# Kernel optimization log

Hardware: AMD Instinct MI355X
Metric: run time of the kernel (lower is better)

The kernel has to match this reference:

```python
import jax, jax.numpy as jnp
import numpy as np

KNOW = 128
EXER_N = 20000
STU_N = 50000
N_EDGES = 1000000
N_EDGES_P = 950000
BATCH = 8192
SOFT_PARA = 0.2
EPS = 1e-8


def setup_inputs() -> dict:
    key = jax.random.key(0)
    ks = jax.random.split(key, 10)
    return {
        'stu_emb': jax.random.normal(ks[0], (STU_N, KNOW), jnp.float32) * 0.1,
        'exer_emb': jax.random.normal(ks[1], (EXER_N, KNOW), jnp.float32) * 0.1,
        'W_ue': jax.random.normal(ks[2], (KNOW, KNOW), jnp.float32) / np.sqrt(KNOW),
        'W_ue_per': jax.random.normal(ks[3], (KNOW, KNOW), jnp.float32) / np.sqrt(KNOW),
        'W_deep': jax.random.normal(ks[4], (KNOW, KNOW), jnp.float32) / np.sqrt(KNOW),
        'src_e': jax.random.randint(ks[5], (N_EDGES,), 0, EXER_N),
        'dst_e': jax.random.randint(ks[6], (N_EDGES,), 0, STU_N),
        'src_p': jax.random.randint(ks[7], (N_EDGES_P,), 0, EXER_N),
        'dst_p': jax.random.randint(ks[8], (N_EDGES_P,), 0, STU_N),
        'stu_id': jax.random.randint(ks[9], (BATCH,), 0, STU_N),
    }


def _graph_layer(exer, W, src, dst):
    # u_from_e: messages flow exercise -> student. Linear transform then mean-aggregate.
    msg = exer[src] @ W                                   # [E_edges, K]
    agg = jax.ops.segment_sum(msg, dst, num_segments=STU_N)
    deg = jax.ops.segment_sum(jnp.ones_like(dst, jnp.float32), dst, num_segments=STU_N)
    return agg / jnp.maximum(deg, 1.0)[:, None]           # [STU_N, K]


def reference(stu_emb, exer_emb, W_ue, W_ue_per, W_deep, src_e, dst_e, src_p, dst_p, stu_id):
    # ExpressionDooubleEva: two parallel graph views
    stu1 = stu_emb + _graph_layer(exer_emb, W_ue, src_e, dst_e)
    stu_per = stu_emb + _graph_layer(exer_emb, W_ue_per, src_p, dst_p)
    # ExpressionSingleEva (u_from_e output is overwritten by u_from_e_deep in source)
    stu2 = stu1 + _graph_layer(exer_emb, W_deep, src_e, dst_e)
    stu2_per = stu_per + _graph_layer(exer_emb, W_deep, src_e, dst_e)

    b1 = stu2[stu_id]          # [B, K]
    b2 = stu2_per[stu_id]      # [B, K]
    n1 = b1 / jnp.linalg.norm(b1, axis=1, keepdims=True)
    n2 = b2 / jnp.linalg.norm(b2, axis=1, keepdims=True)
    sim = (n1 @ n2.T) / SOFT_PARA                         # [B, B]
    # faithful to source: numerator = exp(diag(sim)), denominator = sum of RAW sim row
    diag_exp = jnp.exp(jnp.diagonal(sim))
    row_sum = jnp.sum(sim, axis=1)
    ratio = diag_exp / (row_sum + EPS)
    ssl_loss = jnp.mean(-jnp.log(jnp.maximum(ratio, EPS)))
    return stu2, ssl_loss
```

## Files before the change

### kernel.cpp

```cpp
#include <hip/hip_runtime.h>
#include <math.h>

#define KNOW 128
#define STU_N 50000
#define EXER_N 20000
#define BATCH 8192
#define NE 1000000
#define NEP 950000
#define SOFT_INV 5.0f
#define EPS 1e-8f

#define CAP 64
#define NBIN 256
#define SPB 196
#define SSE 4608
#define SSP 1536
#define P1B 256
#define P1T 1024

typedef unsigned short u16;
typedef unsigned int u32;

typedef __attribute__((ext_vector_type(8))) short bf16x8;
typedef __attribute__((ext_vector_type(4))) float f32x4;

__device__ __forceinline__ u16 f2bf(float f) {
  union { float f; u32 u; } v;
  v.f = f;
  u32 r = (v.u + 0x7FFFu + ((v.u >> 16) & 1u)) >> 16;
  return (u16)r;
}
__device__ __forceinline__ float bflo(u32 u) {
  union { u32 u; float f; } v;
  v.u = u << 16;
  return v.f;
}
__device__ __forceinline__ float bfhi(u32 u) {
  union { u32 u; float f; } v;
  v.u = u & 0xFFFF0000u;
  return v.f;
}
__device__ __forceinline__ float bfu(u16 h) {
  union { u32 u; float f; } v;
  v.u = ((u32)h) << 16;
  return v.f;
}

__global__ void set_flags(const int* __restrict__ stu_id,
                          unsigned char* __restrict__ flag,
                          int* __restrict__ gcur_e, int* __restrict__ gcur_p) {
  int i = blockIdx.x * blockDim.x + threadIdx.x;
  if (i < BATCH) flag[stu_id[i]] = 1;
  if (i < NBIN) {
    gcur_e[i] = i * SSE;
    gcur_p[i] = i * SSP;
  }
}

__global__ __launch_bounds__(P1T) void bin_pass1(
    const int* __restrict__ dst_e, const int* __restrict__ src_e,
    const int* __restrict__ dst_p, const int* __restrict__ src_p,
    const unsigned char* __restrict__ flag, int* __restrict__ gcur_e,
    int* __restrict__ gcur_p, u32* __restrict__ stag_e,
    u32* __restrict__ stag_p) {
  __shared__ int cntE[NBIN], cntP[NBIN];
  __shared__ int baseE[NBIN], baseP[NBIN];
  __shared__ int curE[NBIN], curP[NBIN];
  int t = threadIdx.x;
  if (t < NBIN) {
    cntE[t] = 0;
    cntP[t] = 0;
  }
  __syncthreads();
  int b = blockIdx.x;
  int e0 = (int)((long long)NE * b / P1B);
  int e1 = (int)((long long)NE * (b + 1) / P1B);
  int p0 = (int)((long long)NEP * b / P1B);
  int p1 = (int)((long long)NEP * (b + 1) / P1B);
  for (int i = e0 + t; i < e1; i += P1T) {
    int d = __builtin_nontemporal_load(&dst_e[i]);
    atomicAdd(&cntE[d / SPB], 1);
  }
  for (int i = p0 + t; i < p1; i += P1T) {
    int d = __builtin_nontemporal_load(&dst_p[i]);
    if (flag[d]) atomicAdd(&cntP[d / SPB], 1);
  }
  __syncthreads();
  if (t < NBIN) {
    baseE[t] = atomicAdd(&gcur_e[t], cntE[t]);
    baseP[t] = atomicAdd(&gcur_p[t], cntP[t]);
    curE[t] = 0;
    curP[t] = 0;
  }
  __syncthreads();
  for (int i = e0 + t; i < e1; i += P1T) {
    int d = __builtin_nontemporal_load(&dst_e[i]);
    int s = __builtin_nontemporal_load(&src_e[i]);
    int bin = d / SPB;
    int pos = baseE[bin] + atomicAdd(&curE[bin], 1);
    if (pos < (bin + 1) * SSE)
      stag_e[pos] = ((u32)(d - bin * SPB) << 16) | (u32)s;
  }
  for (int i = p0 + t; i < p1; i += P1T) {
    int d = __builtin_nontemporal_load(&dst_p[i]);
    if (!flag[d]) continue;
    int s = __builtin_nontemporal_load(&src_p[i]);
    int bin = d / SPB;
    int pos = baseP[bin] + atomicAdd(&curP[bin], 1);
    if (pos < (bin + 1) * SSP)
      stag_p[pos] = ((u32)(d - bin * SPB) << 16) | (u32)s;
  }
}

__global__ __launch_bounds__(256) void bin_pass2(
    const u32* __restrict__ stag_e, const u32* __restrict__ stag_p,
    const int* __restrict__ gcur_e, const int* __restrict__ gcur_p,
    u16* __restrict__ bucket_e, u16* __restrict__ bucket_p,
    int* __restrict__ cnt_e, int* __restrict__ cnt_p) {
  __shared__ u16 be[SPB * CAP];
  __shared__ u16 bp[SPB * CAP];
  __shared__ int ce[SPB], cp[SPB];
  int t = threadIdx.x;
  int bin = blockIdx.x;
  for (int i = t; i < SPB; i += 256) {
    ce[i] = 0;
    cp[i] = 0;
  }
  __syncthreads();
  int ne = gcur_e[bin] - bin * SSE;
  if (ne > SSE) ne = SSE;
  int np = gcur_p[bin] - bin * SSP;
  if (np > SSP) np = SSP;
  const u32* se = stag_e + (size_t)bin * SSE;
  for (int i = t; i < ne; i += 256) {
    u32 w = se[i];
    int dl = (int)(w >> 16), s = (int)(w & 0xFFFFu);
    int slot = atomicAdd(&ce[dl], 1);
    if (slot < CAP) be[dl * CAP + slot] = (u16)s;
  }
  const u32* sp = stag_p + (size_t)bin * SSP;
  for (int i = t; i < np; i += 256) {
    u32 w = sp[i];
    int dl = (int)(w >> 16), s = (int)(w & 0xFFFFu);
    int slot = atomicAdd(&cp[dl], 1);
    if (slot < CAP) bp[dl * CAP + slot] = (u16)s;
  }
  __syncthreads();
  int s0 = bin * SPB;
  int nstu = STU_N - s0;
  if (nstu > SPB) nstu = SPB;
  if (nstu <= 0) return;
  int nvec = nstu * CAP * 2 / 16;
  const uint4* bev = (const uint4*)be;
  uint4* ge = (uint4*)(bucket_e + (size_t)s0 * CAP);
  for (int i = t; i < nvec; i += 256) ge[i] = bev[i];
  const uint4* bpv = (const uint4*)bp;
  uint4* gp = (uint4*)(bucket_p + (size_t)s0 * CAP);
  for (int i = t; i < nvec; i += 256) gp[i] = bpv[i];
  for (int i = t; i < nstu; i += 256) {
    cnt_e[s0 + i] = ce[i];
    cnt_p[s0 + i] = cp[i];
  }
}

#define BM_T 80

#define SPL(dh, dl, i, x)                 \
  {                                       \
    u16 _hb = f2bf(x);                    \
    float _hf = bfu(_hb);                 \
    dh[i] = (short)_hb;                   \
    dl[i] = (short)f2bf((x) - _hf);       \
  }

__global__ __launch_bounds__(256) void transform_mfma(
    const float* __restrict__ exer, const float* __restrict__ W_ue,
    const float* __restrict__ W_per, const float* __restrict__ W_deep,
    u16* __restrict__ X_sum, u16* __restrict__ X_per,
    u16* __restrict__ X_deep) {
  __shared__ u16 wt_hi[KNOW * KNOW];
  __shared__ u16 wt_lo[KNOW * KNOW];
  int t = threadIdx.x;
  int which = blockIdx.y;
  u16* outp = (which == 0) ? X_sum : (which == 1) ? X_per : X_deep;

  {
    int c = t & 127;
    int rbase = (t >> 7) * 64;
    int swz = (c & 7) << 4;
    for (int r = rbase; r < rbase + 64; r += 2) {
      float w0, w1;
      if (which == 0) {
        w0 = W_ue[r * KNOW + c] + W_deep[r * KNOW + c];
        w1 = W_ue[(r + 1) * KNOW + c] + W_deep[(r + 1) * KNOW + c];
      } else {
        const float* Ws = (which == 1) ? W_per : W_deep;
        w0 = Ws[r * KNOW + c];
        w1 = Ws[(r + 1) * KNOW + c];
      }
      u16 h0 = f2bf(w0);
      u16 l0 = f2bf(w0 - bfu(h0));
      u16 h1 = f2bf(w1);
      u16 l1 = f2bf(w1 - bfu(h1));
      int bo = c * 256 + ((r * 2) ^ swz);
      *(u32*)((char*)wt_hi + bo) = (u32)h0 | ((u32)h1 << 16);
      *(u32*)((char*)wt_lo + bo) = (u32)l0 | ((u32)l1 << 16);
    }
  }
  __syncthreads();

  int wv = t >> 6;
  int l = t & 63;
  int bn = l & 15;
  int kb = l >> 4;

  bf16x8 bh[2][4], bl[2][4];
#pragma unroll
  for (int nt = 0; nt < 2; ++nt) {
    int n = wv * 32 + nt * 16 + bn;
    int rb = n * 256;
    int swz = (n & 7) << 4;
#pragma unroll
    for (int ks = 0; ks < 4; ++ks) {
      int bo = rb + (((ks * 32 + kb * 8) * 2) ^ swz);
      bh[nt][ks] = *(const bf16x8*)((const char*)wt_hi + bo);
      bl[nt][ks] = *(const bf16x8*)((const char*)wt_lo + bo);
    }
  }

  int row0 = blockIdx.x * BM_T;
#pragma unroll 1
  for (int rt = 0; rt < 5; ++rt) {
    const float* ep = exer + (size_t)(row0 + rt * 16 + bn) * KNOW;
    f32x4 acc0 = {0.f, 0.f, 0.f, 0.f};
    f32x4 acc1 = {0.f, 0.f, 0.f, 0.f};
#pragma unroll
    for (int ks = 0; ks < 4; ++ks) {
      float4 a0 = *(const float4*)(ep + ks * 32 + kb * 8);
      float4 a1 = *(const float4*)(ep + ks * 32 + kb * 8 + 4);
      bf16x8 ah, al;
      SPL(ah, al, 0, a0.x)
      SPL(ah, al, 1, a0.y)
      SPL(ah, al, 2, a0.z)
      SPL(ah, al, 3, a0.w)
      SPL(ah, al, 4, a1.x)
      SPL(ah, al, 5, a1.y)
      SPL(ah, al, 6, a1.z)
      SPL(ah, al, 7, a1.w)
      acc0 = __builtin_amdgcn_mfma_f32_16x16x32_bf16(ah, bh[0][ks], acc0, 0, 0, 0);
      acc0 = __builtin_amdgcn_mfma_f32_16x16x32_bf16(al, bh[0][ks], acc0, 0, 0, 0);
      acc0 = __builtin_amdgcn_mfma_f32_16x16x32_bf16(ah, bl[0][ks], acc0, 0, 0, 0);
      acc1 = __builtin_amdgcn_mfma_f32_16x16x32_bf16(ah, bh[1][ks], acc1, 0, 0, 0);
      acc1 = __builtin_amdgcn_mfma_f32_16x16x32_bf16(al, bh[1][ks], acc1, 0, 0, 0);
      acc1 = __builtin_amdgcn_mfma_f32_16x16x32_bf16(ah, bl[1][ks], acc1, 0, 0, 0);
    }
    int orow = row0 + rt * 16 + kb * 4;
    int oc = wv * 32 + bn;
#pragma unroll
    for (int r = 0; r < 4; ++r) {
      outp[(size_t)(orow + r) * KNOW + oc] = f2bf(acc0[r]);
      outp[(size_t)(orow + r) * KNOW + oc + 16] = f2bf(acc1[r]);
    }
  }
}

__global__ __launch_bounds__(256) void stu2_gather(
    const float* __restrict__ stu_emb, const u16* __restrict__ X_sum,
    const u16* __restrict__ bucket, const int* __restrict__ cnt,
    float* __restrict__ out) {
  int wv = threadIdx.x >> 6;
  int lane = threadIdx.x & 63;
  int s = blockIdx.x * 4 + wv;
  if (s >= STU_N) return;
  int deg = cnt[s];
  int e = (deg < CAP) ? deg : CAP;
  const u16* brow = bucket + (size_t)s * CAP;
  u32 bval = brow[lane];
  float acc0 = 0.f, acc1 = 0.f;
  int i = 0;
  for (; i + 4 <= e; i += 4) {
    int s0 = __builtin_amdgcn_readlane(bval, i);
    int s1 = __builtin_amdgcn_readlane(bval, i + 1);
    int s2 = __builtin_amdgcn_readlane(bval, i + 2);
    int s3 = __builtin_amdgcn_readlane(bval, i + 3);
    u32 w0 = *(const u32*)(X_sum + (size_t)s0 * KNOW + lane * 2);
    u32 w1 = *(const u32*)(X_sum + (size_t)s1 * KNOW + lane * 2);
    u32 w2 = *(const u32*)(X_sum + (size_t)s2 * KNOW + lane * 2);
    u32 w3 = *(const u32*)(X_sum + (size_t)s3 * KNOW + lane * 2);
    acc0 += bflo(w0) + bflo(w1) + bflo(w2) + bflo(w3);
    acc1 += bfhi(w0) + bfhi(w1) + bfhi(w2) + bfhi(w3);
  }
  for (; i < e; ++i) {
    int si = __builtin_amdgcn_readlane(bval, i);
    u32 w0 = *(const u32*)(X_sum + (size_t)si * KNOW + lane * 2);
    acc0 += bflo(w0);
    acc1 += bfhi(w0);
  }
  float inv = 1.0f / fmaxf((float)deg, 1.0f);
  float2 se = *(const float2*)(stu_emb + (size_t)s * KNOW + lane * 2);
  float2 o = {se.x + acc0 * inv, se.y + acc1 * inv};
  *(float2*)(out + (size_t)s * KNOW + lane * 2) = o;
}

__global__ __launch_bounds__(128) void batch_kernel(
    const float* __restrict__ stu_emb, const float* __restrict__ stu2,
    const u16* __restrict__ X_per, const u16* __restrict__ X_deep,
    const u16* __restrict__ bucket_p, const int* __restrict__ cnt_p,
    const u16* __restrict__ bucket_e, const int* __restrict__ cnt_e,
    const int* __restrict__ stu_id, float* __restrict__ n1,
    float* __restrict__ n2, float* __restrict__ diag) {
  __shared__ float red[128];
  int i = blockIdx.x;
  int k = threadIdx.x;
  int sid = stu_id[i];

  int degp = cnt_p[sid];
  int ep = (degp < CAP) ? degp : CAP;
  const u16* brp = bucket_p + (size_t)sid * CAP;
  float accp = 0.0f;
  int j = 0;
  for (; j + 4 <= ep; j += 4) {
    int s0 = brp[j], s1 = brp[j + 1], s2 = brp[j + 2], s3 = brp[j + 3];
    accp += bfu(X_per[(size_t)s0 * KNOW + k]);
    accp += bfu(X_per[(size_t)s1 * KNOW + k]);
    accp += bfu(X_per[(size_t)s2 * KNOW + k]);
    accp += bfu(X_per[(size_t)s3 * KNOW + k]);
  }
  for (; j < ep; ++j) accp += bfu(X_per[(size_t)brp[j] * KNOW + k]);
  accp /= fmaxf((float)degp, 1.0f);

  int degd = cnt_e[sid];
  int ed = (degd < CAP) ? degd : CAP;
  const u16* brd = bucket_e + (size_t)sid * CAP;
  float accd = 0.0f;
  j = 0;
  for (; j + 4 <= ed; j += 4) {
    int s0 = brd[j], s1 = brd[j + 1], s2 = brd[j + 2], s3 = brd[j + 3];
    accd += bfu(X_deep[(size_t)s0 * KNOW + k]);
    accd += bfu(X_deep[(size_t)s1 * KNOW + k]);
    accd += bfu(X_deep[(size_t)s2 * KNOW + k]);
    accd += bfu(X_deep[(size_t)s3 * KNOW + k]);
  }
  for (; j < ed; ++j) accd += bfu(X_deep[(size_t)brd[j] * KNOW + k]);
  accd /= fmaxf((float)degd, 1.0f);

  float b1 = stu2[(size_t)sid * KNOW + k];
  float b2 = stu_emb[(size_t)sid * KNOW + k] + accp + accd;

  red[k] = b1 * b1;
  __syncthreads();
  for (int s = 64; s > 0; s >>= 1) {
    if (k < s) red[k] += red[k + s];
    __syncthreads();
  }
  float norm1 = sqrtf(red[0]);
  __syncthreads();
  red[k] = b2 * b2;
  __syncthreads();
  for (int s = 64; s > 0; s >>= 1) {
    if (k < s) red[k] += red[k + s];
    __syncthreads();
  }
  float norm2 = sqrtf(red[0]);

  float v1 = b1 / norm1;
  float v2 = b2 / norm2;
  n1[(size_t)i * KNOW + k] = v1;
  n2[(size_t)i * KNOW + k] = v2;

  __syncthreads();
  red[k] = v1 * v2;
  __syncthreads();
  for (int s = 64; s > 0; s >>= 1) {
    if (k < s) red[k] += red[k + s];
    __syncthreads();
  }
  if (k == 0) diag[i] = red[0];
}

__global__ __launch_bounds__(128) void s2_reduce(const float* __restrict__ n2,
                                                 float* __restrict__ S2) {
  int k = threadIdx.x;
  int r0 = blockIdx.x * (BATCH / 64);
  float acc = 0.0f;
  for (int r = 0; r < BATCH / 64; ++r) acc += n2[(size_t)(r0 + r) * KNOW + k];
  atomicAdd(&S2[k], acc);
}

#define L2BLKS 64
__global__ __launch_bounds__(256) void loss2(const float* __restrict__ n1,
                                             const float* __restrict__ diag,
                                             const float* __restrict__ S2,
                                             float* __restrict__ loss) {
  __shared__ float s2s[KNOW];
  int t = threadIdx.x;
  if (t < KNOW) s2s[t] = S2[t];
  __syncthreads();
  int wave = t >> 6, lane = t & 63;
  const int rows_per_wave = BATCH / (L2BLKS * 4);
  int r0 = (blockIdx.x * 4 + wave) * rows_per_wave;
  float acc = 0.0f;
  for (int r = r0; r < r0 + rows_per_wave; ++r) {
    float v = n1[(size_t)r * KNOW + lane] * s2s[lane] +
              n1[(size_t)r * KNOW + 64 + lane] * s2s[64 + lane];
#pragma unroll
    for (int off = 32; off > 0; off >>= 1) v += __shfl_down(v, off);
    if (lane == 0) {
      float rs = v * SOFT_INV;
      float dg = diag[r] * SOFT_INV;
      float ratio = expf(dg) / (rs + EPS);
      acc += -logf(fmaxf(ratio, EPS));
    }
  }
  if (lane == 0) atomicAdd(loss, acc);
}

__global__ void finalize_kernel(const float* __restrict__ loss,
                                float* __restrict__ out) {
  out[(size_t)STU_N * KNOW] = loss[0] * (1.0f / (float)BATCH);
}

extern "C" void kernel_launch(void* const* d_in, const int* in_sizes, int n_in,
                              void* d_out, int out_size, void* d_ws,
                              size_t ws_size, hipStream_t stream) {
  const float* stu_emb = (const float*)d_in[0];
  const float* exer_emb = (const float*)d_in[1];
  const float* W_ue = (const float*)d_in[2];
  const float* W_ue_per = (const float*)d_in[3];
  const float* W_deep = (const float*)d_in[4];
  const int* src_e = (const int*)d_in[5];
  const int* dst_e = (const int*)d_in[6];
  const int* src_p = (const int*)d_in[7];
  const int* dst_p = (const int*)d_in[8];
  const int* stu_id = (const int*)d_in[9];
  float* out = (float*)d_out;

  char* wsb = (char*)d_ws;
  float* S2 = (float*)wsb;
  float* loss = S2 + KNOW;
  unsigned char* flag = (unsigned char*)(loss + 1);
  size_t zero_bytes = (size_t)(flag + ((STU_N + 3) & ~3) - (unsigned char*)wsb);
  int* cnt_e = (int*)(flag + ((STU_N + 3) & ~3));
  int* cnt_p = cnt_e + STU_N;
  int* gcur_e = cnt_p + STU_N;
  int* gcur_p = gcur_e + NBIN;
  u16* X_sum = (u16*)(gcur_p + NBIN);
  u16* X_per = X_sum + (size_t)EXER_N * KNOW;
  u16* X_deep = X_per + (size_t)EXER_N * KNOW;
  u16* bucket_e = X_deep + (size_t)EXER_N * KNOW;
  u16* bucket_p = bucket_e + (size_t)STU_N * CAP;
  u32* stag_e = (u32*)(bucket_p + (size_t)STU_N * CAP);
  u32* stag_p = stag_e + (size_t)NBIN * SSE;
  float* n1 = (float*)(stag_p + (size_t)NBIN * SSP);
  float* n2 = n1 + (size_t)BATCH * KNOW;
  float* diag = n2 + (size_t)BATCH * KNOW;

  hipMemsetAsync(d_ws, 0, zero_bytes, stream);

  set_flags<<<(BATCH + 255) / 256, 256, 0, stream>>>(stu_id, flag, gcur_e,
                                                     gcur_p);

  {
    dim3 grid(EXER_N / BM_T, 3);
    transform_mfma<<<grid, 256, 0, stream>>>(exer_emb, W_ue, W_ue_per, W_deep,
                                             X_sum, X_per, X_deep);
  }

  bin_pass1<<<P1B, P1T, 0, stream>>>(dst_e, src_e, dst_p, src_p, flag, gcur_e,
                                     gcur_p, stag_e, stag_p);

  bin_pass2<<<NBIN, 256, 0, stream>>>(stag_e, stag_p, gcur_e, gcur_p, bucket_e,
                                      bucket_p, cnt_e, cnt_p);

  stu2_gather<<<(STU_N + 3) / 4, 256, 0, stream>>>(stu_emb, X_sum, bucket_e,
                                                   cnt_e, out);

  batch_kernel<<<BATCH, 128, 0, stream>>>(stu_emb, out, X_per, X_deep,
                                          bucket_p, cnt_p, bucket_e, cnt_e,
                                          stu_id, n1, n2, diag);

  s2_reduce<<<64, 128, 0, stream>>>(n2, S2);

  loss2<<<L2BLKS, 256, 0, stream>>>(n1, diag, S2, loss);

  finalize_kernel<<<1, 1, 0, stream>>>(loss, out);
}
```

Measured before the change: 284.3 us.

## Pre-split exercise and weight matrices into bf16 hi/lo in a separate prep kernel

A new prep_split kernel converts exer_emb and the three weight matrices into bf16 hi/lo halves once, storing them in global scratch in a transposed weight layout. The weight buffers alias the staging, n1 and n2 regions, which are only written later in the same stream. The transform kernel no longer uses LDS or redoes the split per block. Each 512-thread block now runs all three weight variants over the same 80 rows, so exer rows are read from the pre-split buffers. The aim is to avoid redundant float-to-bf16 splitting and the threefold float exer reads, at the cost of an extra launch and extra global write/read traffic for the split arrays.

```diff
diff --git a/kernel.cpp b/kernel.cpp
--- a/kernel.cpp
+++ b/kernel.cpp
@@ -54,6 +54,98 @@
   if (i < NBIN) {
     gcur_e[i] = i * SSE;
     gcur_p[i] = i * SSP;
+  }
+}
+
+__global__ __launch_bounds__(256) void prep_split(
+    const float* __restrict__ exer, const float* __restrict__ W_ue,
+    const float* __restrict__ W_per, const float* __restrict__ W_deep,
+    u16* __restrict__ Ah, u16* __restrict__ Al, u16* __restrict__ WTh,
+    u16* __restrict__ WTl) {
+  int b = blockIdx.x;
+  if (b < 3) {
+    int t = threadIdx.x;
+    int n = t & 127;
+    int kh = (t >> 7) * 64;
+    const float* W0 = (b == 0) ? W_ue : (b == 1) ? W_per : W_deep;
+#pragma unroll 1
+    for (int kc = 0; kc < 64; kc += 8) {
+      u16 hi[8], lo[8];
+#pragma unroll
+      for (int j = 0; j < 8; ++j) {
+        int k = kh + kc + j;
+        float x = W0[k * KNOW + n];
+        if (b == 0) x += W_deep[k * KNOW + n];
+        u16 h = f2bf(x);
+        hi[j] = h;
+        lo[j] = f2bf(x - bfu(h));
+      }
+      size_t base = ((size_t)b * KNOW + n) * KNOW + kh + kc;
+      uint4 H = {(u32)hi[0] | ((u32)hi[1] << 16), (u32)hi[2] | ((u32)hi[3] << 16),
+                 (u32)hi[4] | ((u32)hi[5] << 16), (u32)hi[6] | ((u32)hi[7] << 16)};
+      uint4 L = {(u32)lo[0] | ((u32)lo[1] << 16), (u32)lo[2] | ((u32)lo[3] << 16),
+                 (u32)lo[4] | ((u32)lo[5] << 16), (u32)lo[6] | ((u32)lo[7] << 16)};
+      *(uint4*)(WTh + base) = H;
+      *(uint4*)(WTl + base) = L;
+    }
+  } else {
+    size_t i = ((size_t)(b - 3) * 256 + threadIdx.x) * 4;
+    float4 v = *(const float4*)(exer + i);
+    u16 h0 = f2bf(v.x), h1 = f2bf(v.y), h2 = f2bf(v.z), h3 = f2bf(v.w);
+    ushort4 H = {h0, h1, h2, h3};
+    ushort4 L = {f2bf(v.x - bfu(h0)), f2bf(v.y - bfu(h1)), f2bf(v.z - bfu(h2)),
+                 f2bf(v.w - bfu(h3))};
+    *(ushort4*)(Ah + i) = H;
+    *(ushort4*)(Al + i) = L;
+  }
+}
+
+#define BM_T 80
+
+__global__ __launch_bounds__(512) void transform_mfma(
+    const u16* __restrict__ Ah, const u16* __restrict__ Al,
+    const u16* __restrict__ WTh, const u16* __restrict__ WTl,
+    u16* __restrict__ X_sum, u16* __restrict__ X_per,
+    u16* __restrict__ X_deep) {
+  int t = threadIdx.x;
+  int wv = t >> 6;
+  int l = t & 63;
+  int bn = l & 15;
+  int kb = l >> 4;
+  int row0 = blockIdx.x * BM_T;
+  int n = wv * 16 + bn;
+
+#pragma unroll 1
+  for (int which = 0; which < 3; ++which) {
+    u16* outp = (which == 0) ? X_sum : (which == 1) ? X_per : X_deep;
+    const u16* wth = WTh + (size_t)which * KNOW * KNOW;
+    const u16* wtl = WTl + (size_t)which * KNOW * KNOW;
+    bf16x8 bh[4], bl[4];
+#pragma unroll
+    for (int ks = 0; ks < 4; ++ks) {
+      int off = n * KNOW + ks * 32 + kb * 8;
+      bh[ks] = *(const bf16x8*)(wth + off);
+      bl[ks] = *(const bf16x8*)(wtl + off);
+    }
+#pragma unroll 1
+    for (int rt = 0; rt < 5; ++rt) {
+      int row = row0 + rt * 16 + bn;
+      const u16* ap = Ah + (size_t)row * KNOW + kb * 8;
+      const u16* alp = Al + (size_t)row * KNOW + kb * 8;
+      f32x4 acc = {0.f, 0.f, 0.f, 0.f};
+#pragma unroll
+      for (int ks = 0; ks < 4; ++ks) {
+        bf16x8 af = *(const bf16x8*)(ap + ks * 32);
+        bf16x8 lf = *(const bf16x8*)(alp + ks * 32);
+        acc = __builtin_amdgcn_mfma_f32_16x16x32_bf16(af, bh[ks], acc, 0, 0, 0);
+        acc = __builtin_amdgcn_mfma_f32_16x16x32_bf16(lf, bh[ks], acc, 0, 0, 0);
+        acc = __builtin_amdgcn_mfma_f32_16x16x32_bf16(af, bl[ks], acc, 0, 0, 0);
+      }
+      int orow = row0 + rt * 16 + kb * 4;
+#pragma unroll
+      for (int r = 0; r < 4; ++r)
+        outp[(size_t)(orow + r) * KNOW + n] = f2bf(acc[r]);
+    }
   }
 }
 
@@ -160,107 +252,6 @@
   for (int i = t; i < nstu; i += 256) {
     cnt_e[s0 + i] = ce[i];
     cnt_p[s0 + i] = cp[i];
-  }
-}
-
-#define BM_T 80
-
-#define SPL(dh, dl, i, x)                 \
-  {                                       \
-    u16 _hb = f2bf(x);                    \
-    float _hf = bfu(_hb);                 \
-    dh[i] = (short)_hb;                   \
-    dl[i] = (short)f2bf((x) - _hf);       \
-  }
-
-__global__ __launch_bounds__(256) void transform_mfma(
-    const float* __restrict__ exer, const float* __restrict__ W_ue,
-    const float* __restrict__ W_per, const float* __restrict__ W_deep,
-    u16* __restrict__ X_sum, u16* __restrict__ X_per,
-    u16* __restrict__ X_deep) {
-  __shared__ u16 wt_hi[KNOW * KNOW];
-  __shared__ u16 wt_lo[KNOW * KNOW];
-  int t = threadIdx.x;
-  int which = blockIdx.y;
-  u16* outp = (which == 0) ? X_sum : (which == 1) ? X_per : X_deep;
-
-  {
-    int c = t & 127;
-    int rbase = (t >> 7) * 64;
-    int swz = (c & 7) << 4;
-    for (int r = rbase; r < rbase + 64; r += 2) {
-      float w0, w1;
-      if (which == 0) {
-        w0 = W_ue[r * KNOW + c] + W_deep[r * KNOW + c];
-        w1 = W_ue[(r + 1) * KNOW + c] + W_deep[(r + 1) * KNOW + c];
-      } else {
-        const float* Ws = (which == 1) ? W_per : W_deep;
-        w0 = Ws[r * KNOW + c];
-        w1 = Ws[(r + 1) * KNOW + c];
-      }
-      u16 h0 = f2bf(w0);
-      u16 l0 = f2bf(w0 - bfu(h0));
-      u16 h1 = f2bf(w1);
-      u16 l1 = f2bf(w1 - bfu(h1));
-      int bo = c * 256 + ((r * 2) ^ swz);
-      *(u32*)((char*)wt_hi + bo) = (u32)h0 | ((u32)h1 << 16);
-      *(u32*)((char*)wt_lo + bo) = (u32)l0 | ((u32)l1 << 16);
-    }
-  }
-  __syncthreads();
-
-  int wv = t >> 6;
-  int l = t & 63;
-  int bn = l & 15;
-  int kb = l >> 4;
-
-  bf16x8 bh[2][4], bl[2][4];
-#pragma unroll
-  for (int nt = 0; nt < 2; ++nt) {
-    int n = wv * 32 + nt * 16 + bn;
-    int rb = n * 256;
-    int swz = (n & 7) << 4;
-#pragma unroll
-    for (int ks = 0; ks < 4; ++ks) {
-      int bo = rb + (((ks * 32 + kb * 8) * 2) ^ swz);
-      bh[nt][ks] = *(const bf16x8*)((const char*)wt_hi + bo);
-      bl[nt][ks] = *(const bf16x8*)((const char*)wt_lo + bo);
-    }
-  }
-
-  int row0 = blockIdx.x * BM_T;
-#pragma unroll 1
-  for (int rt = 0; rt < 5; ++rt) {
-    const float* ep = exer + (size_t)(row0 + rt * 16 + bn) * KNOW;
-    f32x4 acc0 = {0.f, 0.f, 0.f, 0.f};
-    f32x4 acc1 = {0.f, 0.f, 0.f, 0.f};
-#pragma unroll
-    for (int ks = 0; ks < 4; ++ks) {
-      float4 a0 = *(const float4*)(ep + ks * 32 + kb * 8);
-      float4 a1 = *(const float4*)(ep + ks * 32 + kb * 8 + 4);
-      bf16x8 ah, al;
-      SPL(ah, al, 0, a0.x)
-      SPL(ah, al, 1, a0.y)
-      SPL(ah, al, 2, a0.z)
-      SPL(ah, al, 3, a0.w)
-      SPL(ah, al, 4, a1.x)
-      SPL(ah, al, 5, a1.y)
-      SPL(ah, al, 6, a1.z)
-      SPL(ah, al, 7, a1.w)
-      acc0 = __builtin_amdgcn_mfma_f32_16x16x32_bf16(ah, bh[0][ks], acc0, 0, 0, 0);
-      acc0 = __builtin_amdgcn_mfma_f32_16x16x32_bf16(al, bh[0][ks], acc0, 0, 0, 0);
-      acc0 = __builtin_amdgcn_mfma_f32_16x16x32_bf16(ah, bl[0][ks], acc0, 0, 0, 0);
-      acc1 = __builtin_amdgcn_mfma_f32_16x16x32_bf16(ah, bh[1][ks], acc1, 0, 0, 0);
-      acc1 = __builtin_amdgcn_mfma_f32_16x16x32_bf16(al, bh[1][ks], acc1, 0, 0, 0);
-      acc1 = __builtin_amdgcn_mfma_f32_16x16x32_bf16(ah, bl[1][ks], acc1, 0, 0, 0);
-    }
-    int orow = row0 + rt * 16 + kb * 4;
-    int oc = wv * 32 + bn;
-#pragma unroll
-    for (int r = 0; r < 4; ++r) {
-      outp[(size_t)(orow + r) * KNOW + oc] = f2bf(acc0[r]);
-      outp[(size_t)(orow + r) * KNOW + oc + 16] = f2bf(acc1[r]);
-    }
   }
 }
 
@@ -455,16 +446,21 @@
   float* n2 = n1 + (size_t)BATCH * KNOW;
   float* diag = n2 + (size_t)BATCH * KNOW;
 
+  u16* Ah = (u16*)stag_e;
+  u16* Al = (u16*)n1;
+  u16* WTh = Al + (size_t)EXER_N * KNOW;
+  u16* WTl = WTh + (size_t)3 * KNOW * KNOW;
+
   hipMemsetAsync(d_ws, 0, zero_bytes, stream);
 
   set_flags<<<(BATCH + 255) / 256, 256, 0, stream>>>(stu_id, flag, gcur_e,
                                                      gcur_p);
 
-  {
-    dim3 grid(EXER_N / BM_T, 3);
-    transform_mfma<<<grid, 256, 0, stream>>>(exer_emb, W_ue, W_ue_per, W_deep,
-                                             X_sum, X_per, X_deep);
-  }
+  prep_split<<<3 + EXER_N * KNOW / 1024, 256, 0, stream>>>(
+      exer_emb, W_ue, W_ue_per, W_deep, Ah, Al, WTh, WTl);
+
+  transform_mfma<<<EXER_N / BM_T, 512, 0, stream>>>(Ah, Al, WTh, WTl, X_sum,
+                                                    X_per, X_deep);
 
   bin_pass1<<<P1B, P1T, 0, stream>>>(dst_e, src_e, dst_p, src_p, flag, gcur_e,
                                      gcur_p, stag_e, stag_p);
```

New measurement: 298.3 us. 1.05x slower.
